# Kernel optimization log

Hardware: AMD Instinct MI355X
Metric: run time of the kernel (lower is better)

## Reference

```python
import jax, jax.numpy as jnp
import numpy as np

V, E, H = 50000, 256, 512
BS, SEQ = 64, 200


def setup_inputs() -> dict:
    key = jax.random.key(0)
    ks = jax.random.split(key, 16)
    s = 0.05
    return {
        "input_idx": jax.random.randint(ks[0], (BS,), 0, V),
        "encoded": jax.random.normal(ks[1], (BS, SEQ, 2 * H), jnp.float32),
        "encoded_idx": jax.random.randint(ks[2], (BS, SEQ), 0, V),
        "prev_state": jax.random.normal(ks[3], (BS, H), jnp.float32),
        "weighted": jax.random.normal(ks[4], (BS, 1, 2 * H), jnp.float32),
        "order": 1,
        "embed_W": jax.random.normal(ks[5], (V, E), jnp.float32) * s,
        "Wih": jax.random.normal(ks[6], (3 * H, E + 2 * H), jnp.float32) * s,
        "Whh": jax.random.normal(ks[7], (3 * H, H), jnp.float32) * s,
        "bih": jax.random.normal(ks[8], (3 * H,), jnp.float32) * s,
        "bhh": jax.random.normal(ks[9], (3 * H,), jnp.float32) * s,
        "Ws_W": jax.random.normal(ks[10], (H, 2 * H), jnp.float32) * s,
        "Ws_b": jax.random.normal(ks[11], (H,), jnp.float32) * s,
        "Wo_W": jax.random.normal(ks[12], (V, H), jnp.float32) * s,
        "Wo_b": jax.random.normal(ks[13], (V,), jnp.float32) * s,
        "Wc_W": jax.random.normal(ks[14], (H, 2 * H), jnp.float32) * s,
        "Wc_b": jax.random.normal(ks[15], (H,), jnp.float32) * s,
    }


def reference(input_idx, encoded, encoded_idx, prev_state, weighted, order,
              embed_W, Wih, Whh, bih, bhh, Ws_W, Ws_b, Wo_W, Wo_b, Wc_W, Wc_b):
    bs, seq, _ = encoded.shape
    hidden = Ws_W.shape[0]
    vocab = Wo_W.shape[0]

    if order == 0:
        prev_state = encoded[:, 1] @ Ws_W.T + Ws_b            # [bs, H]
        weighted = jnp.zeros((bs, 1, 2 * hidden), encoded.dtype)

    # GRU single step (batch_first, seq len 1)
    x = jnp.concatenate([embed_W[input_idx], weighted[:, 0, :]], axis=1)  # [bs, E+2H]
    gi = x @ Wih.T + bih                                       # [bs, 3H]
    gh = prev_state @ Whh.T + bhh                              # [bs, 3H]
    i_r, i_z, i_n = jnp.split(gi, 3, axis=1)
    h_r, h_z, h_n = jnp.split(gh, 3, axis=1)
    r = jax.nn.sigmoid(i_r + h_r)
    z = jax.nn.sigmoid(i_z + h_z)
    n = jnp.tanh(i_n + r * h_n)
    state = (1.0 - z) * n + z * prev_state                     # [bs, H]

    # generate and copy scores
    score_g = state @ Wo_W.T + Wo_b                            # [bs, V]
    sc = jnp.tanh(encoded @ Wc_W.T + Wc_b)                     # [bs, seq, H]
    score_c = jnp.einsum('bsh,bh->bs', sc, state)              # [bs, seq]
    enc_mask = jnp.where(encoded_idx == 0, -1000.0, 0.0).astype(score_c.dtype)
    score_c = jnp.tanh(score_c + enc_mask)

    probs = jax.nn.softmax(jnp.concatenate([score_g, score_c], axis=1), axis=1)
    prob_g = probs[:, :vocab]                                  # [bs, V]
    prob_c = probs[:, vocab:]                                  # [bs, seq]

    # scatter-add copy probs into vocab slots
    prob_c_to_g = jnp.zeros((bs, vocab), probs.dtype).at[
        jnp.arange(bs)[:, None], encoded_idx].add(prob_c)
    out = (prob_g + prob_c_to_g)[:, None, :]                   # [bs, 1, V]

    # selective-read attention over positions matching input token
    m = (encoded_idx == input_idx[:, None]).astype(encoded.dtype)  # [bs, seq]
    ssum = m.sum(axis=1, keepdims=True)
    m = jnp.where(ssum > 1, m / ssum, m)
    attn = (prob_c * m)[:, None, :]                            # [bs, 1, seq]
    weighted_out = attn @ encoded                              # [bs, 1, 2H]

    return out, state, weighted_out
```

## Files before the change

### kernel.cpp

```cpp
#include <hip/hip_runtime.h>

#define V 50000
#define E_DIM 256
#define H_DIM 512
#define H2 1024
#define G3 1536
#define BSZ 64
#define SEQ 200
#define KX 1280
#define MROWS 12800
#define NBLK_WO 782

#define XBF_OFF   0
#define H0_OFF    40960
#define H0BF_OFF  73728
#define GI_OFF    90112
#define GH_OFF    188416
#define STBF_OFF  286720
#define WCBF_OFF  303104
#define SC_OFF    565248
#define REDG_OFF  616448
#define RED_OFF   716544
#define ENCBF_OFF 716672

#define OUT_STATE 3200000
#define OUT_W     3232768

typedef __attribute__((ext_vector_type(8))) short bf16x8;
typedef __attribute__((ext_vector_type(4))) float f32x4;

__device__ __forceinline__ float sigmf(float x) { return 1.f / (1.f + __expf(-x)); }

__device__ __forceinline__ ushort f2bf(float f) {
  uint u = __float_as_uint(f);
  uint r = (u + 0x7FFFu + ((u >> 16) & 1u)) >> 16;
  return (ushort)r;
}

__device__ __forceinline__ float tanhfast(float x) {
  float xc = fminf(15.f, fmaxf(-15.f, x));
  float e = __expf(2.f * xc);
  return (e - 1.f) * __builtin_amdgcn_rcpf(e + 1.f);
}

__device__ __forceinline__ bf16x8 cvt8(float4 a, float4 b) {
  union { bf16x8 v; uint u[4]; } r;
  asm("v_cvt_pk_bf16_f32 %0, %1, %2" : "=v"(r.u[0]) : "v"(a.x), "v"(a.y));
  asm("v_cvt_pk_bf16_f32 %0, %1, %2" : "=v"(r.u[1]) : "v"(a.z), "v"(a.w));
  asm("v_cvt_pk_bf16_f32 %0, %1, %2" : "=v"(r.u[2]) : "v"(b.x), "v"(b.y));
  asm("v_cvt_pk_bf16_f32 %0, %1, %2" : "=v"(r.u[3]) : "v"(b.z), "v"(b.w));
  return r.v;
}

__device__ __forceinline__ void gload16(const void* g, void* l) {
  __builtin_amdgcn_global_load_lds(
      (__attribute__((address_space(1))) void*)(g),
      (__attribute__((address_space(3))) void*)(l), 16, 0, 0);
}

__global__ void kprep(const float* __restrict__ Wc_W, ushort* __restrict__ Wc_bf,
                      const float* __restrict__ encoded, ushort* __restrict__ enc_bf,
                      const int* __restrict__ input_idx,
                      const float* __restrict__ prev_state, const float* __restrict__ weighted,
                      const int* __restrict__ order_p, const float* __restrict__ embed_W,
                      const float* __restrict__ Ws_W, const float* __restrict__ Ws_b,
                      ushort* __restrict__ x_bf, float* __restrict__ h0,
                      ushort* __restrict__ h0_bf) {
  int bid = blockIdx.x, tid = threadIdx.x;
  if (bid < 512) {
    int i = bid * 256 + tid;
    float4 v = ((const float4*)Wc_W)[i];
    ushort4 o;
    o.x = f2bf(v.x); o.y = f2bf(v.y); o.z = f2bf(v.z); o.w = f2bf(v.w);
    ((ushort4*)Wc_bf)[i] = o;
    return;
  }
  if (bid < 3712) {
    int base = (bid - 512) * 1024;
#pragma unroll
    for (int j = 0; j < 4; ++j) {
      int i = base + j * 256 + tid;
      float4 v = ((const float4*)encoded)[i];
      ushort4 o;
      o.x = f2bf(v.x); o.y = f2bf(v.y); o.z = f2bf(v.z); o.w = f2bf(v.w);
      ((ushort4*)enc_bf)[i] = o;
    }
    return;
  }
  int b = bid - 3712;
  int order = order_p[0];
  int idx = input_idx[b];
  x_bf[b * KX + tid] = f2bf(embed_W[(size_t)idx * E_DIM + tid]);
  if (order != 0) {
    for (int j = tid; j < H2; j += 256) x_bf[b * KX + E_DIM + j] = f2bf(weighted[b * H2 + j]);
    for (int j = tid; j < H_DIM; j += 256) {
      float v = prev_state[b * H_DIM + j];
      h0[b * H_DIM + j] = v;
      h0_bf[b * H_DIM + j] = f2bf(v);
    }
  } else {
    for (int j = tid; j < H2; j += 256) x_bf[b * KX + E_DIM + j] = 0;
    const float* er = encoded + ((size_t)b * SEQ + 1) * H2;
    for (int j = tid; j < H_DIM; j += 256) {
      float acc = Ws_b[j];
      const float* wr = Ws_W + (size_t)j * H2;
      for (int k = 0; k < H2; ++k) acc = fmaf(er[k], wr[k], acc);
      h0[b * H_DIM + j] = acc;
      h0_bf[b * H_DIM + j] = f2bf(acc);
    }
  }
}

__device__ __forceinline__ void gemm_small(const ushort* __restrict__ Abf,
                                           const float* __restrict__ W,
                                           const float* __restrict__ bias,
                                           float* __restrict__ out, int N, int kdim,
                                           int bid) {
  int tid = threadIdx.x;
  int lane = tid & 63, wv = tid >> 6;
  int l15 = lane & 15, lg = lane >> 4;
  int n0 = (bid * 4 + wv) * 16;
  int col = n0 + l15;
  bool valid = col < N;
  int colc = valid ? col : N - 1;
  f32x4 acc[4];
#pragma unroll
  for (int mt = 0; mt < 4; ++mt) acc[mt] = (f32x4){0.f, 0.f, 0.f, 0.f};
  const float* wrow = W + (size_t)colc * kdim + lg * 8;
  const ushort* arow = Abf + (size_t)l15 * kdim + lg * 8;
#pragma unroll 4
  for (int k0 = 0; k0 < kdim; k0 += 32) {
    float4 w0 = *(const float4*)(wrow + k0);
    float4 w1 = *(const float4*)(wrow + k0 + 4);
    bf16x8 bf = cvt8(w0, w1);
#pragma unroll
    for (int mt = 0; mt < 4; ++mt) {
      bf16x8 af = *(const bf16x8*)(arow + (size_t)mt * 16 * kdim + k0);
      acc[mt] = __builtin_amdgcn_mfma_f32_16x16x32_bf16(af, bf, acc[mt], 0, 0, 0);
    }
  }
  float bv = bias[colc];
  if (valid) {
#pragma unroll
    for (int mt = 0; mt < 4; ++mt)
#pragma unroll
      for (int r = 0; r < 4; ++r)
        out[(size_t)(mt * 16 + lg * 4 + r) * N + col] = acc[mt][r] + bv;
  }
}

__global__ __launch_bounds__(256) void mfma_gates(const ushort* __restrict__ x_bf,
                                                  const float* __restrict__ Wih,
                                                  const float* __restrict__ bih,
                                                  const ushort* __restrict__ h0_bf,
                                                  const float* __restrict__ Whh,
                                                  const float* __restrict__ bhh,
                                                  float* __restrict__ gi, float* __restrict__ gh) {
  if (blockIdx.y == 0)
    gemm_small(x_bf, Wih, bih, gi, G3, KX, blockIdx.x);
  else
    gemm_small(h0_bf, Whh, bhh, gh, G3, H_DIM, blockIdx.x);
}

__global__ void k2_gru(const float* __restrict__ gi, const float* __restrict__ gh,
                       const float* __restrict__ h0, float* __restrict__ state_out,
                       ushort* __restrict__ state_bf) {
  int b = blockIdx.x, j = threadIdx.x;
  float ir = gi[b * G3 + j], iz = gi[b * G3 + H_DIM + j], inn = gi[b * G3 + 2 * H_DIM + j];
  float hr = gh[b * G3 + j], hz = gh[b * G3 + H_DIM + j], hn = gh[b * G3 + 2 * H_DIM + j];
  float r = sigmf(ir + hr);
  float z = sigmf(iz + hz);
  float n = tanhf(inn + r * hn);
  float st = (1.f - z) * n + z * h0[b * H_DIM + j];
  state_out[b * H_DIM + j] = st;
  state_bf[b * H_DIM + j] = f2bf(st);
}

__global__ __launch_bounds__(256, 2) void wo_stage(const ushort* __restrict__ state_bf,
                                                   const float* __restrict__ Wo_W,
                                                   const float* __restrict__ Wo_b,
                                                   float* __restrict__ out,
                                                   float* __restrict__ redg) {
  __shared__ char shmem[81920];
  int tid = threadIdx.x, lane = tid & 63, wv = tid >> 6;
  int l15 = lane & 15, lg = lane >> 4;
  int bid = blockIdx.x;
  int col0 = bid * 64 + wv * 16 + l15;
  bool v0ok = col0 < V;
  int cc0 = v0ok ? col0 : V - 1;
  const float* s0 = Wo_W + (size_t)cc0 * H_DIM + lg * 8;

#pragma unroll
  for (int j = 0; j < 16; ++j) {
    int slot = wv * 16 + j;
    int mf = slot >> 4, it = slot & 15;
    gload16(state_bf + (size_t)(mf * 16 + l15) * H_DIM + it * 32 + lg * 8,
            shmem + slot * 1024);
  }
  {
    char* d_ = shmem + 65536 + wv * 2048;
    gload16(s0, d_);
    gload16(s0 + 4, d_ + 1024);
  }
  __syncthreads();

  f32x4 acc[4];
#pragma unroll
  for (int mt = 0; mt < 4; ++mt) acc[mt] = (f32x4){0.f, 0.f, 0.f, 0.f};

#pragma unroll 1
  for (int it = 0; it < 16; ++it) {
    int cur = it & 1;
    if (it < 15) {
      char* d_ = shmem + 65536 + (cur ^ 1) * 8192 + wv * 2048;
      gload16(s0 + (it + 1) * 32, d_);
      gload16(s0 + (it + 1) * 32 + 4, d_ + 1024);
      asm volatile("s_waitcnt vmcnt(2)" ::: "memory");
    } else {
      asm volatile("s_waitcnt vmcnt(0)" ::: "memory");
    }
    const char* wb = shmem + 65536 + cur * 8192 + wv * 2048;
    float4 w00 = *(const float4*)(wb + lane * 16);
    float4 w01 = *(const float4*)(wb + 1024 + lane * 16);
    bf16x8 wf0 = cvt8(w00, w01);
    bf16x8 af0 = *(const bf16x8*)(shmem + (0 * 16 + it) * 1024 + lane * 16);
    bf16x8 af1 = *(const bf16x8*)(shmem + (1 * 16 + it) * 1024 + lane * 16);
    bf16x8 af2 = *(const bf16x8*)(shmem + (2 * 16 + it) * 1024 + lane * 16);
    bf16x8 af3 = *(const bf16x8*)(shmem + (3 * 16 + it) * 1024 + lane * 16);
    acc[0] = __builtin_amdgcn_mfma_f32_16x16x32_bf16(af0, wf0, acc[0], 0, 0, 0);
    acc[1] = __builtin_amdgcn_mfma_f32_16x16x32_bf16(af1, wf0, acc[1], 0, 0, 0);
    acc[2] = __builtin_amdgcn_mfma_f32_16x16x32_bf16(af2, wf0, acc[2], 0, 0, 0);
    acc[3] = __builtin_amdgcn_mfma_f32_16x16x32_bf16(af3, wf0, acc[3], 0, 0, 0);
  }

  float bv0 = Wo_b[cc0];
#pragma unroll
  for (int mt = 0; mt < 4; ++mt)
#pragma unroll
    for (int r = 0; r < 4; ++r) {
      size_t row = (size_t)(mt * 16 + lg * 4 + r) * V;
      if (v0ok) out[row + col0] = acc[mt][r] + bv0;
    }
  float* smw = (float*)(shmem + 65536 + wv * 2048);
  float* ssw = smw + 64;
#pragma unroll
  for (int mt = 0; mt < 4; ++mt)
#pragma unroll
    for (int r = 0; r < 4; ++r) {
      float a0 = v0ok ? acc[mt][r] + bv0 : -1e30f;
      float mx = a0;
#pragma unroll
      for (int off = 1; off < 16; off <<= 1) mx = fmaxf(mx, __shfl_xor(mx, off, 64));
      float e = v0ok ? __expf(a0 - mx) : 0.f;
#pragma unroll
      for (int off = 1; off < 16; off <<= 1) e += __shfl_xor(e, off, 64);
      if (l15 == 0) {
        smw[mt * 16 + lg * 4 + r] = mx;
        ssw[mt * 16 + lg * 4 + r] = e;
      }
    }
  __syncthreads();
  if (tid < 64) {
    float M = -1e30f, S = 0.f;
#pragma unroll
    for (int w = 0; w < 4; ++w) {
      const float* smx = (const float*)(shmem + 65536 + w * 2048);
      float m2 = smx[tid], s2 = smx[64 + tid];
      float mn = fmaxf(M, m2);
      S = S * __expf(M - mn) + s2 * __expf(m2 - mn);
      M = mn;
    }
    redg[((size_t)tid * NBLK_WO + bid) * 2] = M;
    redg[((size_t)tid * NBLK_WO + bid) * 2 + 1] = S;
  }
}

__global__ __launch_bounds__(256) void k4_mfma9(const ushort* __restrict__ enc_bf,
                                                const ushort* __restrict__ Wc_bf,
                                                const float* __restrict__ Wc_b,
                                                const float* __restrict__ state,
                                                float* __restrict__ scpart) {
  __shared__ char lds[2][24576];
  __shared__ float sred[4][64];
  int tid = threadIdx.x, lane = tid & 63, wv = tid >> 6;
  int l15 = lane & 15, lg = lane >> 4;
  int bid = blockIdx.x;
  int mtile = bid >> 2, ntile = bid & 3;
  int m0 = mtile * 64, n0 = ntile * 128;

  const ushort* asrc = enc_bf + (size_t)(m0 + wv * 16 + l15) * H2 + lg * 8;
  const ushort* bsrc0 = Wc_bf + (size_t)(n0 + (wv * 2 + 0) * 16 + l15) * H2 + lg * 8;
  const ushort* bsrc1 = Wc_bf + (size_t)(n0 + (wv * 2 + 1) * 16 + l15) * H2 + lg * 8;

  f32x4 acc[4][2];
#pragma unroll
  for (int mf = 0; mf < 4; ++mf)
#pragma unroll
    for (int nf = 0; nf < 2; ++nf) acc[mf][nf] = (f32x4){0.f, 0.f, 0.f, 0.f};

#define STG(buf, it) do {                                              \
    char* d_ = &lds[buf][0];                                           \
    gload16(asrc + (it) * 64,       d_ + (wv * 2 + 0) * 1024);         \
    gload16(asrc + (it) * 64 + 32,  d_ + (wv * 2 + 1) * 1024);         \
    gload16(bsrc0 + (it) * 64,      d_ + 8192 + (wv * 4 + 0) * 1024);  \
    gload16(bsrc0 + (it) * 64 + 32, d_ + 8192 + (wv * 4 + 1) * 1024);  \
    gload16(bsrc1 + (it) * 64,      d_ + 8192 + (wv * 4 + 2) * 1024);  \
    gload16(bsrc1 + (it) * 64 + 32, d_ + 8192 + (wv * 4 + 3) * 1024);  \
  } while (0)

  STG(0, 0);
  __syncthreads();
#pragma unroll 1
  for (int it = 0; it < 16; ++it) {
    int cur = it & 1;
    if (it < 15) STG(cur ^ 1, it + 1);
    const char* base = &lds[cur][0];
#pragma unroll
    for (int ks = 0; ks < 2; ++ks) {
      bf16x8 b0 = *(const bf16x8*)(base + 8192 + (wv * 4 + ks) * 1024 + lane * 16);
      bf16x8 b1 = *(const bf16x8*)(base + 8192 + (wv * 4 + 2 + ks) * 1024 + lane * 16);
#pragma unroll
      for (int mf = 0; mf < 4; ++mf) {
        bf16x8 a = *(const bf16x8*)(base + (mf * 2 + ks) * 1024 + lane * 16);
        acc[mf][0] = __builtin_amdgcn_mfma_f32_16x16x32_bf16(a, b0, acc[mf][0], 0, 0, 0);
        acc[mf][1] = __builtin_amdgcn_mfma_f32_16x16x32_bf16(a, b1, acc[mf][1], 0, 0, 0);
      }
    }
    __syncthreads();
  }
#undef STG

  float pv[4][4];
#pragma unroll
  for (int mf = 0; mf < 4; ++mf)
#pragma unroll
    for (int r = 0; r < 4; ++r) pv[mf][r] = 0.f;
#pragma unroll
  for (int nfl = 0; nfl < 2; ++nfl) {
    int n = n0 + (wv * 2 + nfl) * 16 + l15;
    float bias = Wc_b[n];
#pragma unroll
    for (int mf = 0; mf < 4; ++mf) {
      int mrow = m0 + mf * 16 + lg * 4;
#pragma unroll
      for (int r = 0; r < 4; ++r) {
        int b = (mrow + r) / SEQ;
        pv[mf][r] += tanhfast(acc[mf][nfl][r] + bias) * state[b * H_DIM + n];
      }
    }
  }
#pragma unroll
  for (int off = 1; off < 16; off <<= 1)
#pragma unroll
    for (int mf = 0; mf < 4; ++mf)
#pragma unroll
      for (int r = 0; r < 4; ++r) pv[mf][r] += __shfl_xor(pv[mf][r], off, 64);
  if (l15 == 0) {
#pragma unroll
    for (int mf = 0; mf < 4; ++mf)
#pragma unroll
      for (int r = 0; r < 4; ++r) sred[wv][mf * 16 + lg * 4 + r] = pv[mf][r];
  }
  __syncthreads();
  if (tid < 64) {
    float s = sred[0][tid] + sred[1][tid] + sred[2][tid] + sred[3][tid];
    scpart[(size_t)ntile * MROWS + m0 + tid] = s;
  }
}

__global__ void kred(const float* __restrict__ redg, const float* __restrict__ scpart,
                     const int* __restrict__ eidx, float* __restrict__ red) {
  int b = blockIdx.x, tid = threadIdx.x;
  float m = -1e30f, s = 0.f;
  for (int i = tid; i < NBLK_WO; i += 256) {
    float m2 = redg[((size_t)b * NBLK_WO + i) * 2];
    float s2 = redg[((size_t)b * NBLK_WO + i) * 2 + 1];
    float mn = fmaxf(m, m2);
    s = s * __expf(m - mn) + s2 * __expf(m2 - mn);
    m = mn;
  }
  for (int i = tid; i < SEQ; i += 256) {
    int idx = b * SEQ + i;
    int ei = eidx[idx];
    float scv = scpart[idx] + scpart[MROWS + idx] + scpart[2 * MROWS + idx] +
                scpart[3 * MROWS + idx];
    float sc = tanhf(scv + (ei == 0 ? -1000.f : 0.f));
    float mn = fmaxf(m, sc);
    s = s * __expf(m - mn) + __expf(sc - mn);
    m = mn;
  }
  __shared__ float ms[256], ssh[256];
  ms[tid] = m; ssh[tid] = s;
  __syncthreads();
  for (int off = 128; off > 0; off >>= 1) {
    if (tid < off) {
      float m2 = ms[tid + off], s2 = ssh[tid + off];
      float mn = fmaxf(ms[tid], m2);
      ssh[tid] = ssh[tid] * __expf(ms[tid] - mn) + s2 * __expf(m2 - mn);
      ms[tid] = mn;
    }
    __syncthreads();
  }
  if (tid == 0) {
    red[b * 2] = ms[0];
    red[b * 2 + 1] = ssh[0];
  }
}

__global__ void k7_probs(float* __restrict__ sg, const float* __restrict__ red) {
  int i = blockIdx.x * 256 + threadIdx.x;
  int b = i / 12500;
  float mm = red[b * 2], rd = 1.f / red[b * 2 + 1];
  float4* p = (float4*)sg;
  float4 v = p[i];
  v.x = __expf(v.x - mm) * rd;
  v.y = __expf(v.y - mm) * rd;
  v.z = __expf(v.z - mm) * rd;
  v.w = __expf(v.w - mm) * rd;
  p[i] = v;
}

__global__ void k8_copy(const float* __restrict__ scpart, const int* __restrict__ eidx,
                        const int* __restrict__ input_idx, const float* __restrict__ red,
                        const float* __restrict__ encoded, float* __restrict__ out,
                        float* __restrict__ wout) {
  int b = blockIdx.x, tid = threadIdx.x;
  __shared__ float att_s[SEQ];
  __shared__ int cnt_s[256];
  float mm = red[b * 2], rd = 1.f / red[b * 2 + 1];
  int inp = input_idx[b];
  int cnt = 0;
  for (int s = tid; s < SEQ; s += 256) {
    int idx = b * SEQ + s;
    int ei = eidx[idx];
    float scv = scpart[idx] + scpart[MROWS + idx] + scpart[2 * MROWS + idx] +
                scpart[3 * MROWS + idx];
    float sc = tanhf(scv + (ei == 0 ? -1000.f : 0.f));
    float p = __expf(sc - mm) * rd;
    bool mt = (ei == inp);
    att_s[s] = mt ? p : 0.f;
    cnt += mt ? 1 : 0;
    atomicAdd(&out[(size_t)b * V + ei], p);
  }
  cnt_s[tid] = cnt;
  __syncthreads();
  for (int off = 128; off > 0; off >>= 1) {
    if (tid < off) cnt_s[tid] += cnt_s[tid + off];
    __syncthreads();
  }
  int c = cnt_s[0];
  float scale = (c > 1) ? 1.f / (float)c : 1.f;
  float w0 = 0, w1 = 0, w2 = 0, w3 = 0;
  for (int s = 0; s < SEQ; ++s) {
    float a = att_s[s];
    if (a != 0.f) {
      const float* er = encoded + ((size_t)b * SEQ + s) * H2;
      w0 += a * er[tid];
      w1 += a * er[tid + 256];
      w2 += a * er[tid + 512];
      w3 += a * er[tid + 768];
    }
  }
  wout[b * H2 + tid] = w0 * scale;
  wout[b * H2 + tid + 256] = w1 * scale;
  wout[b * H2 + tid + 512] = w2 * scale;
  wout[b * H2 + tid + 768] = w3 * scale;
}

extern "C" void kernel_launch(void* const* d_in, const int* in_sizes, int n_in,
                              void* d_out, int out_size, void* d_ws, size_t ws_size,
                              hipStream_t stream) {
  const int* input_idx = (const int*)d_in[0];
  const float* encoded = (const float*)d_in[1];
  const int* encoded_idx = (const int*)d_in[2];
  const float* prev_state = (const float*)d_in[3];
  const float* weighted = (const float*)d_in[4];
  const int* order_p = (const int*)d_in[5];
  const float* embed_W = (const float*)d_in[6];
  const float* Wih = (const float*)d_in[7];
  const float* Whh = (const float*)d_in[8];
  const float* bih = (const float*)d_in[9];
  const float* bhh = (const float*)d_in[10];
  const float* Ws_W = (const float*)d_in[11];
  const float* Ws_b = (const float*)d_in[12];
  const float* Wo_W = (const float*)d_in[13];
  const float* Wo_b = (const float*)d_in[14];
  const float* Wc_W = (const float*)d_in[15];
  const float* Wc_b = (const float*)d_in[16];

  float* ws = (float*)d_ws;
  float* out = (float*)d_out;
  ushort* x_bf = (ushort*)(ws + XBF_OFF);
  float* h0 = ws + H0_OFF;
  ushort* h0_bf = (ushort*)(ws + H0BF_OFF);
  float* gi = ws + GI_OFF;
  float* gh = ws + GH_OFF;
  ushort* state_bf = (ushort*)(ws + STBF_OFF);
  ushort* Wc_bf = (ushort*)(ws + WCBF_OFF);
  float* scpart = ws + SC_OFF;
  float* redg = ws + REDG_OFF;
  float* red = ws + RED_OFF;
  ushort* enc_bf = (ushort*)(ws + ENCBF_OFF);
  float* state = out + OUT_STATE;
  float* wout = out + OUT_W;

  kprep<<<3776, 256, 0, stream>>>(Wc_W, Wc_bf, encoded, enc_bf, input_idx, prev_state,
                                  weighted, order_p, embed_W, Ws_W, Ws_b, x_bf, h0, h0_bf);
  mfma_gates<<<dim3(24, 2), 256, 0, stream>>>(x_bf, Wih, bih, h0_bf, Whh, bhh, gi, gh);
  k2_gru<<<64, 512, 0, stream>>>(gi, gh, h0, state, state_bf);
  wo_stage<<<NBLK_WO, 256, 0, stream>>>(state_bf, Wo_W, Wo_b, out, redg);
  k4_mfma9<<<800, 256, 0, stream>>>(enc_bf, Wc_bf, Wc_b, state, scpart);
  kred<<<64, 256, 0, stream>>>(redg, scpart, encoded_idx, red);
  k7_probs<<<3125, 256, 0, stream>>>(out, red);
  k8_copy<<<64, 256, 0, stream>>>(scpart, encoded_idx, input_idx, red, encoded, out, wout);
}
```

Baseline: 164.0 us.

## Stream activations with weights in double-buffered K-chunks for Wo GEMM

The Wo projection kernel no longer preloads the full 64x512 bf16 state tile (64 KB of LDS) before computing. It now streams both the activation and the weight slices in 64-wide K chunks through a 48 KB double-buffered LDS ring, with block-wide barriers between iterations. This cuts LDS use per block, which allows more resident blocks and removes the long upfront activation load. In exchange it adds a __syncthreads per iteration and reloads activations per chunk instead of keeping them resident.

```diff
diff --git a/kernel.cpp b/kernel.cpp
--- a/kernel.cpp
+++ b/kernel.cpp
@@ -176,87 +176,81 @@
   state_bf[b * H_DIM + j] = f2bf(st);
 }
 
-__global__ __launch_bounds__(256, 2) void wo_stage(const ushort* __restrict__ state_bf,
-                                                   const float* __restrict__ Wo_W,
-                                                   const float* __restrict__ Wo_b,
-                                                   float* __restrict__ out,
-                                                   float* __restrict__ redg) {
-  __shared__ char shmem[81920];
+__global__ __launch_bounds__(256) void wo_m97(const ushort* __restrict__ state_bf,
+                                              const float* __restrict__ Wo_W,
+                                              const float* __restrict__ Wo_b,
+                                              float* __restrict__ out,
+                                              float* __restrict__ redg) {
+  __shared__ char lds[2][24576];
+  __shared__ float sm[4][64], ss[4][64];
   int tid = threadIdx.x, lane = tid & 63, wv = tid >> 6;
   int l15 = lane & 15, lg = lane >> 4;
   int bid = blockIdx.x;
-  int col0 = bid * 64 + wv * 16 + l15;
-  bool v0ok = col0 < V;
-  int cc0 = v0ok ? col0 : V - 1;
-  const float* s0 = Wo_W + (size_t)cc0 * H_DIM + lg * 8;
-
-#pragma unroll
-  for (int j = 0; j < 16; ++j) {
-    int slot = wv * 16 + j;
-    int mf = slot >> 4, it = slot & 15;
-    gload16(state_bf + (size_t)(mf * 16 + l15) * H_DIM + it * 32 + lg * 8,
-            shmem + slot * 1024);
-  }
-  {
-    char* d_ = shmem + 65536 + wv * 2048;
-    gload16(s0, d_);
-    gload16(s0 + 4, d_ + 1024);
-  }
+  int n0 = bid * 64;
+  int colw = n0 + wv * 16 + l15;
+  bool vok = colw < V;
+  int ccw = vok ? colw : V - 1;
+  const ushort* asrc = state_bf + (size_t)(wv * 16 + l15) * H_DIM + lg * 8;
+  const float* wsrc = Wo_W + (size_t)ccw * H_DIM + lg * 8;
+
+  f32x4 acc[4];
+#pragma unroll
+  for (int mf = 0; mf < 4; ++mf) acc[mf] = (f32x4){0.f, 0.f, 0.f, 0.f};
+
+#define STG(buf, it) do {                                               \
+    char* d_ = &lds[buf][0];                                            \
+    gload16(asrc + (it) * 64,      d_ + (wv * 2 + 0) * 1024);           \
+    gload16(asrc + (it) * 64 + 32, d_ + (wv * 2 + 1) * 1024);           \
+    gload16(wsrc + (it) * 64,      d_ + 8192 + (wv * 4 + 0) * 1024);    \
+    gload16(wsrc + (it) * 64 + 4,  d_ + 8192 + (wv * 4 + 1) * 1024);    \
+    gload16(wsrc + (it) * 64 + 32, d_ + 8192 + (wv * 4 + 2) * 1024);    \
+    gload16(wsrc + (it) * 64 + 36, d_ + 8192 + (wv * 4 + 3) * 1024);    \
+  } while (0)
+
+  STG(0, 0);
   __syncthreads();
-
-  f32x4 acc[4];
-#pragma unroll
-  for (int mt = 0; mt < 4; ++mt) acc[mt] = (f32x4){0.f, 0.f, 0.f, 0.f};
-
 #pragma unroll 1
-  for (int it = 0; it < 16; ++it) {
+  for (int it = 0; it < 8; ++it) {
     int cur = it & 1;
-    if (it < 15) {
-      char* d_ = shmem + 65536 + (cur ^ 1) * 8192 + wv * 2048;
-      gload16(s0 + (it + 1) * 32, d_);
-      gload16(s0 + (it + 1) * 32 + 4, d_ + 1024);
-      asm volatile("s_waitcnt vmcnt(2)" ::: "memory");
-    } else {
-      asm volatile("s_waitcnt vmcnt(0)" ::: "memory");
-    }
-    const char* wb = shmem + 65536 + cur * 8192 + wv * 2048;
-    float4 w00 = *(const float4*)(wb + lane * 16);
-    float4 w01 = *(const float4*)(wb + 1024 + lane * 16);
-    bf16x8 wf0 = cvt8(w00, w01);
-    bf16x8 af0 = *(const bf16x8*)(shmem + (0 * 16 + it) * 1024 + lane * 16);
-    bf16x8 af1 = *(const bf16x8*)(shmem + (1 * 16 + it) * 1024 + lane * 16);
-    bf16x8 af2 = *(const bf16x8*)(shmem + (2 * 16 + it) * 1024 + lane * 16);
-    bf16x8 af3 = *(const bf16x8*)(shmem + (3 * 16 + it) * 1024 + lane * 16);
-    acc[0] = __builtin_amdgcn_mfma_f32_16x16x32_bf16(af0, wf0, acc[0], 0, 0, 0);
-    acc[1] = __builtin_amdgcn_mfma_f32_16x16x32_bf16(af1, wf0, acc[1], 0, 0, 0);
-    acc[2] = __builtin_amdgcn_mfma_f32_16x16x32_bf16(af2, wf0, acc[2], 0, 0, 0);
-    acc[3] = __builtin_amdgcn_mfma_f32_16x16x32_bf16(af3, wf0, acc[3], 0, 0, 0);
-  }
-
-  float bv0 = Wo_b[cc0];
-#pragma unroll
-  for (int mt = 0; mt < 4; ++mt)
+    if (it < 7) STG(cur ^ 1, it + 1);
+    const char* base = &lds[cur][0];
+#pragma unroll
+    for (int ks = 0; ks < 2; ++ks) {
+      float4 w0 = *(const float4*)(base + 8192 + (wv * 4 + ks * 2 + 0) * 1024 + lane * 16);
+      float4 w1 = *(const float4*)(base + 8192 + (wv * 4 + ks * 2 + 1) * 1024 + lane * 16);
+      bf16x8 wf = cvt8(w0, w1);
+#pragma unroll
+      for (int mf = 0; mf < 4; ++mf) {
+        bf16x8 a = *(const bf16x8*)(base + (mf * 2 + ks) * 1024 + lane * 16);
+        acc[mf] = __builtin_amdgcn_mfma_f32_16x16x32_bf16(a, wf, acc[mf], 0, 0, 0);
+      }
+    }
+    __syncthreads();
+  }
+#undef STG
+
+  float bv = Wo_b[ccw];
+#pragma unroll
+  for (int mf = 0; mf < 4; ++mf)
 #pragma unroll
     for (int r = 0; r < 4; ++r) {
-      size_t row = (size_t)(mt * 16 + lg * 4 + r) * V;
-      if (v0ok) out[row + col0] = acc[mt][r] + bv0;
-    }
-  float* smw = (float*)(shmem + 65536 + wv * 2048);
-  float* ssw = smw + 64;
-#pragma unroll
-  for (int mt = 0; mt < 4; ++mt)
+      size_t row = (size_t)(mf * 16 + lg * 4 + r) * V;
+      if (vok) out[row + colw] = acc[mf][r] + bv;
+    }
+#pragma unroll
+  for (int mf = 0; mf < 4; ++mf)
 #pragma unroll
     for (int r = 0; r < 4; ++r) {
-      float a0 = v0ok ? acc[mt][r] + bv0 : -1e30f;
+      float a0 = vok ? acc[mf][r] + bv : -1e30f;
       float mx = a0;
 #pragma unroll
       for (int off = 1; off < 16; off <<= 1) mx = fmaxf(mx, __shfl_xor(mx, off, 64));
-      float e = v0ok ? __expf(a0 - mx) : 0.f;
+      float e = vok ? __expf(a0 - mx) : 0.f;
 #pragma unroll
       for (int off = 1; off < 16; off <<= 1) e += __shfl_xor(e, off, 64);
       if (l15 == 0) {
-        smw[mt * 16 + lg * 4 + r] = mx;
-        ssw[mt * 16 + lg * 4 + r] = e;
+        sm[wv][mf * 16 + lg * 4 + r] = mx;
+        ss[wv][mf * 16 + lg * 4 + r] = e;
       }
     }
   __syncthreads();
@@ -264,8 +258,7 @@
     float M = -1e30f, S = 0.f;
 #pragma unroll
     for (int w = 0; w < 4; ++w) {
-      const float* smx = (const float*)(shmem + 65536 + w * 2048);
-      float m2 = smx[tid], s2 = smx[64 + tid];
+      float m2 = sm[w][tid], s2 = ss[w][tid];
       float mn = fmaxf(M, m2);
       S = S * __expf(M - mn) + s2 * __expf(m2 - mn);
       M = mn;
@@ -508,7 +501,7 @@
                                   weighted, order_p, embed_W, Ws_W, Ws_b, x_bf, h0, h0_bf);
   mfma_gates<<<dim3(24, 2), 256, 0, stream>>>(x_bf, Wih, bih, h0_bf, Whh, bhh, gi, gh);
   k2_gru<<<64, 512, 0, stream>>>(gi, gh, h0, state, state_bf);
-  wo_stage<<<NBLK_WO, 256, 0, stream>>>(state_bf, Wo_W, Wo_b, out, redg);
+  wo_m97<<<NBLK_WO, 256, 0, stream>>>(state_bf, Wo_W, Wo_b, out, redg);
   k4_mfma9<<<800, 256, 0, stream>>>(enc_bf, Wc_bf, Wc_b, state, scpart);
   kred<<<64, 256, 0, stream>>>(redg, scpart, encoded_idx, red);
   k7_probs<<<3125, 256, 0, stream>>>(out, red);
```

New measurement: 164.2 us. Within noise of the previous version (+0.1%).
